# Kernel optimization log

Hardware: AMD Instinct MI355X
Metric: run time of the kernel (lower is better)

The kernel has to match this reference:

```python
import jax, jax.numpy as jnp
import numpy as np

N, E, F_IN, HID, G = 20000, 320000, 128, 128, 64
H, D = 8, 32  # TransformerConv heads, per-head dim


def setup_inputs() -> dict:
    key = jax.random.key(0)
    ks = jax.random.split(key, 24)
    def w(k, i, o):
        return (jax.random.normal(k, (i, o), jnp.float32) / np.float32(np.sqrt(i)))
    def b(k, o):
        return jax.random.normal(k, (o,), jnp.float32) * 0.01
    inp = {
        'x': jax.random.normal(ks[0], (N, F_IN), jnp.float32),
        'edge_index': jax.random.randint(ks[1], (2, E), 0, N, jnp.int32),
        'batch': jnp.sort(jax.random.randint(ks[2], (N,), 0, G, jnp.int32)),
        # SAGEConv 1: 128 -> 128 (lin_l has bias, lin_r none)
        's1_wl': w(ks[3], 128, 128), 's1_bl': b(ks[4], 128), 's1_wr': w(ks[5], 128, 128),
        # SAGEConv 2: 128 -> 256
        's2_wl': w(ks[6], 128, 256), 's2_bl': b(ks[7], 256), 's2_wr': w(ks[8], 128, 256),
        # TransformerConv 1: 256 -> 8*32
        't1_wq': w(ks[9], 256, 256), 't1_bq': b(ks[10], 256),
        't1_wk': w(ks[11], 256, 256), 't1_bk': b(ks[12], 256),
        't1_wv': w(ks[13], 256, 256), 't1_bv': b(ks[14], 256),
        't1_ws': w(ks[15], 256, 256), 't1_bs': b(ks[16], 256),
        # TransformerConv 2
        't2_wq': w(ks[17], 256, 256), 't2_bq': b(ks[18], 256),
        't2_wk': w(ks[19], 256, 256), 't2_bk': b(ks[20], 256),
        't2_wv': w(ks[21], 256, 256), 't2_bv': b(ks[22], 256),
        't2_ws': w(ks[23], 256, 256), 't2_bs': b(jax.random.fold_in(key, 100), 256),
        # proj MLP: 256 -> 512 -> HID
        'p1_w': w(jax.random.fold_in(key, 101), 256, 512), 'p1_b': b(jax.random.fold_in(key, 102), 512),
        'p2_w': w(jax.random.fold_in(key, 103), 512, HID), 'p2_b': b(jax.random.fold_in(key, 104), HID),
    }
    return inp


def _sage(x, src, dst, wl, bl, wr):
    # PyG SAGEConv (aggr='mean'): lin_l(mean_j x_j) + lin_r(x_i)
    s = jax.ops.segment_sum(x[src], dst, num_segments=N)           # [N,F]
    cnt = jax.ops.segment_sum(jnp.ones((src.shape[0], 1), x.dtype), dst, num_segments=N)
    mean = s / jnp.maximum(cnt, 1.0)
    return mean @ wl + bl + x @ wr


def _tconv(x, src, dst, wq, bq, wk, bk, wv, bv, ws, bs):
    # PyG TransformerConv(256, 32, heads=8): per-edge attention + skip
    q = (x @ wq + bq).reshape(N, H, D)
    k = (x @ wk + bk).reshape(N, H, D)
    v = (x @ wv + bv).reshape(N, H, D)
    logits = jnp.einsum('ehd,ehd->eh', q[dst], k[src]) / np.float32(np.sqrt(D))  # [E,H]
    m = jax.ops.segment_max(logits, dst, num_segments=N)           # [N,H]
    p = jnp.exp(logits - m[dst])
    denom = jax.ops.segment_sum(p, dst, num_segments=N)
    p = p / denom[dst]                                              # softmax per target node per head
    agg = jax.ops.segment_sum(p[:, :, None] * v[src], dst, num_segments=N)  # [N,H,D]
    return agg.reshape(N, H * D) + x @ ws + bs


def reference(x, edge_index, batch, s1_wl, s1_bl, s1_wr, s2_wl, s2_bl, s2_wr,
              t1_wq, t1_bq, t1_wk, t1_bk, t1_wv, t1_bv, t1_ws, t1_bs,
              t2_wq, t2_bq, t2_wk, t2_bk, t2_wv, t2_bv, t2_ws, t2_bs,
              p1_w, p1_b, p2_w, p2_b):
    src, dst = edge_index[0], edge_index[1]
    h = jax.nn.relu(_sage(x, src, dst, s1_wl, s1_bl, s1_wr))
    h = jax.nn.relu(_sage(h, src, dst, s2_wl, s2_bl, s2_wr))
    h = jax.nn.relu(_tconv(h, src, dst, t1_wq, t1_bq, t1_wk, t1_bk, t1_wv, t1_bv, t1_ws, t1_bs))
    h = jax.nn.relu(_tconv(h, src, dst, t2_wq, t2_bq, t2_wk, t2_bk, t2_wv, t2_bv, t2_ws, t2_bs))
    # proj: ReLU -> Linear(256,512) -> ReLU -> Linear(512,HID) -> Sigmoid
    h = jax.nn.relu(h)
    h = jax.nn.relu(h @ p1_w + p1_b)
    h = jax.nn.sigmoid(h @ p2_w + p2_b)
    return jax.ops.segment_max(h, batch, num_segments=G)            # global_max_pool [G,HID]
```

## Files before the change

kernel.cpp:

```cpp
#include <hip/hip_runtime.h>
#include <hip/hip_bf16.h>
#include <hip/hip_fp16.h>
#include <math.h>

#define NN 20000
#define EE 320000
#define GG 64
#define CH 16

typedef __hip_bfloat16 bf16;
typedef __attribute__((ext_vector_type(8))) short short8;
typedef __attribute__((ext_vector_type(4))) float f32x4;
typedef __attribute__((ext_vector_type(4))) unsigned int uint4v;
typedef __attribute__((ext_vector_type(2))) unsigned int uint2v;
typedef __attribute__((ext_vector_type(2))) _Float16 half2v;
typedef unsigned int uint;
typedef unsigned short ushort;

__device__ __forceinline__ float bfr2f(ushort u) {
    union { uint i; float f; } c; c.i = ((uint)u) << 16; return c.f;
}
__device__ __forceinline__ ushort f2bfr(float f) {
    bf16 h = __float2bfloat16(f);
    return *(ushort*)&h;
}

__device__ __forceinline__ float dot2acc(uint a, uint b, float c) {
#if __has_builtin(__builtin_amdgcn_fdot2)
    return __builtin_amdgcn_fdot2(__builtin_bit_cast(half2v, a),
                                  __builtin_bit_cast(half2v, b), c, false);
#else
    half2v ha = __builtin_bit_cast(half2v, a);
    half2v hb = __builtin_bit_cast(half2v, b);
    return c + (float)ha.x * (float)hb.x + (float)ha.y * (float)hb.y;
#endif
}

__device__ __forceinline__ void load_lds16(const void* g, void* l) {
    __builtin_amdgcn_global_load_lds(
        (const __attribute__((address_space(1))) unsigned int*)g,
        (__attribute__((address_space(3))) unsigned int*)l, 16, 0, 0);
}

#define PREP_CONV  1250
#define PREP_TP    (PREP_CONV + 800)
#define PREP_BIAS  (PREP_TP + 8)
#define PREP_OUTZ  (PREP_BIAS + 32)
#define PREP_COUNT (PREP_OUTZ + 1250)

__global__ __launch_bounds__(256) void prep_kernel(
    const float* x, bf16* xm1,
    const float* s1_wr, const float* s1_wl, const float* s2_wr, const float* s2_wl,
    const float* t1_wq, const float* t1_wk, const float* t1_wv, const float* t1_ws,
    const float* t2_wq, const float* t2_wk, const float* t2_wv, const float* t2_ws,
    const float* p1_w, const float* p2_w,
    bf16* w1cat, bf16* w2cat, bf16* qw1, bf16* qw2, bf16* p1t, bf16* p2t,
    const float* b1q, const float* b1k, const float* b1v, const float* b1s,
    const float* b2q, const float* b2k, const float* b2v, const float* b2s,
    float* qb1, float* qb2,
    float* pool_out,
    const int* dst, int* cnt) {
    __shared__ float tile[32][33];
    int bid = blockIdx.x;
    int tid = threadIdx.x;
    if (bid < PREP_CONV) {
        int g = bid * 256 + tid;
        int row = g >> 4;
        int col = (g & 15) * 8;
        f32x4 a = *(const f32x4*)(x + (size_t)row * 128 + col);
        f32x4 b = *(const f32x4*)(x + (size_t)row * 128 + col + 4);
        short8 v;
        v[0] = (short)f2bfr(a.x); v[1] = (short)f2bfr(a.y);
        v[2] = (short)f2bfr(a.z); v[3] = (short)f2bfr(a.w);
        v[4] = (short)f2bfr(b.x); v[5] = (short)f2bfr(b.y);
        v[6] = (short)f2bfr(b.z); v[7] = (short)f2bfr(b.w);
        *(short8*)(xm1 + (size_t)row * 256 + col) = v;
    } else if (bid < PREP_TP) {
        int tb = bid - PREP_CONV;
        const float* W; bf16* Wt; int KW, NW, KT, KO, lt;
        const float* t1w[4] = {t1_wq, t1_wk, t1_wv, t1_ws};
        const float* t2w[4] = {t2_wq, t2_wk, t2_wv, t2_ws};
        if (tb < 16)       { W = s1_wr; Wt = w1cat; KW = 128; NW = 128; KT = 256; KO = 0;   lt = tb; }
        else if (tb < 32)  { W = s1_wl; Wt = w1cat; KW = 128; NW = 128; KT = 256; KO = 128; lt = tb - 16; }
        else if (tb < 64)  { W = s2_wr; Wt = w2cat; KW = 128; NW = 256; KT = 256; KO = 0;   lt = tb - 32; }
        else if (tb < 96)  { W = s2_wl; Wt = w2cat; KW = 128; NW = 256; KT = 256; KO = 128; lt = tb - 64; }
        else if (tb < 352) { int m = (tb - 96) >> 6;  W = t1w[m]; Wt = qw1 + m * 65536; KW = 256; NW = 256; KT = 256; KO = 0; lt = (tb - 96) & 63; }
        else if (tb < 608) { int m = (tb - 352) >> 6; W = t2w[m]; Wt = qw2 + m * 65536; KW = 256; NW = 256; KT = 256; KO = 0; lt = (tb - 352) & 63; }
        else if (tb < 736) { W = p1_w; Wt = p1t; KW = 256; NW = 512; KT = 256; KO = 0; lt = tb - 608; }
        else               { W = p2_w; Wt = p2t; KW = 512; NW = 128; KT = 512; KO = 0; lt = tb - 736; }
        int ntiles_n = NW >> 5;
        int k0 = (lt / ntiles_n) * 32;
        int n0 = (lt % ntiles_n) * 32;
        int tx = tid & 31, ty = tid >> 5;
        #pragma unroll
        for (int r = 0; r < 4; r++)
            tile[ty + 8 * r][tx] = W[(size_t)(k0 + ty + 8 * r) * NW + n0 + tx];
        __syncthreads();
        #pragma unroll
        for (int r = 0; r < 4; r++)
            Wt[(size_t)(n0 + ty + 8 * r) * KT + KO + k0 + tx] =
                __float2bfloat16(tile[tx][ty + 8 * r]);
    } else if (bid < PREP_BIAS) {
        int i = (bid - PREP_TP) * 256 + tid;
        if (i < 2048) {
            float* d = (i < 1024) ? qb1 : qb2;
            int j = i & 1023;
            const float* s;
            if (i < 1024) s = (j < 256) ? b1q : (j < 512) ? b1k : (j < 768) ? b1v : b1s;
            else          s = (j < 256) ? b2q : (j < 512) ? b2k : (j < 768) ? b2v : b2s;
            d[j] = s[j & 255];
        }
    } else if (bid < PREP_OUTZ) {
        int i = (bid - PREP_BIAS) * 256 + tid;
        if (i < GG * 128) pool_out[i] = 0.f;
    } else {
        int e = (bid - PREP_OUTZ) * 256 + tid;
        if (e < EE) atomicAdd(&cnt[dst[e]], 1);
    }
}

__global__ __launch_bounds__(1024) void scan_kernel(int* __restrict__ cnt,
                                                    int* __restrict__ off, int n) {
    __shared__ int wsum[16];
    __shared__ int carry_s;
    int tid = threadIdx.x;
    int lane = tid & 63, wid = tid >> 6;
    if (tid == 0) { carry_s = 0; off[0] = 0; }
    __syncthreads();
    for (int base = 0; base < n; base += 1024) {
        int idx = base + tid;
        int val = (idx < n) ? cnt[idx] : 0;
        int x = val;
        #pragma unroll
        for (int s = 1; s < 64; s <<= 1) {
            int y = __shfl_up(x, s, 64);
            if (lane >= s) x += y;
        }
        if (lane == 63) wsum[wid] = x;
        __syncthreads();
        if (tid == 0) {
            int c = carry_s;
            #pragma unroll
            for (int w = 0; w < 16; w++) { int t = wsum[w]; wsum[w] = c; c += t; }
            carry_s = c;
        }
        __syncthreads();
        int incl = wsum[wid] + x;
        if (idx < n) {
            off[idx + 1] = incl;
            cnt[idx] = incl - val;
        }
        __syncthreads();
    }
}

__global__ __launch_bounds__(256) void fill_kernel(const int* __restrict__ src,
                                                   const int* __restrict__ dst,
                                                   int* __restrict__ cursor,
                                                   int* __restrict__ csr_src, int E) {
    int e = blockIdx.x * 256 + threadIdx.x;
    if (e < E) {
        int p = atomicAdd(&cursor[dst[e]], 1);
        csr_src[p] = src[e];
    }
}

__global__ __launch_bounds__(256) void mean2_kernel(const bf16* __restrict__ x, int xstride,
                                                    const int* __restrict__ off,
                                                    const int* __restrict__ csr_src,
                                                    bf16* __restrict__ outp, int ostride) {
    int node = blockIdx.x * 4 + (threadIdx.x >> 6);
    int l = threadIdx.x & 63;
    int el = l >> 5;
    int dp = l & 31;
    int e0 = off[node], e1 = off[node + 1];
    float s0 = 0.f, s1 = 0.f, s2 = 0.f, s3 = 0.f;
    for (int e = e0; e < e1; e += 8) {
        uint2v a[4];
        #pragma unroll
        for (int j = 0; j < 4; j++) {
            int ee = e + j * 2 + el;
            int sa = csr_src[min(ee, e1 - 1)];
            uint2v v = *(const uint2v*)(x + (size_t)sa * xstride + dp * 4);
            uint m = (ee < e1) ? 0xffffffffu : 0u;
            a[j].x = v.x & m;
            a[j].y = v.y & m;
        }
        #pragma unroll
        for (int j = 0; j < 4; j++) {
            union { uint i; float f; } t;
            t.i = a[j].x << 16;         s0 += t.f;
            t.i = a[j].x & 0xffff0000u; s1 += t.f;
            t.i = a[j].y << 16;         s2 += t.f;
            t.i = a[j].y & 0xffff0000u; s3 += t.f;
        }
    }
    s0 += __shfl_xor(s0, 32);
    s1 += __shfl_xor(s1, 32);
    s2 += __shfl_xor(s2, 32);
    s3 += __shfl_xor(s3, 32);
    if (el == 0) {
        int deg = e1 - e0;
        float inv = (deg > 0) ? 1.f / (float)deg : 0.f;
        uint2v r;
        r.x = ((uint)f2bfr(s1 * inv) << 16) | (uint)f2bfr(s0 * inv);
        r.y = ((uint)f2bfr(s3 * inv) << 16) | (uint)f2bfr(s2 * inv);
        *(uint2v*)(outp + (size_t)node * ostride + dp * 4) = r;
    }
}

template <int MODE, int TM>
__global__ __launch_bounds__(256, (TM == 128) ? 4 : 5)
void gemm_kernel(const bf16* __restrict__ A,
                 const bf16* __restrict__ Wt,
                 const float* __restrict__ bias,
                 void* __restrict__ Cv,
                 int M, int K, int N, int cstride,
                 const int* __restrict__ batch,
                 float* __restrict__ pool_out) {
    constexpr int NT = (TM == 128) ? 4 : 2;
    constexpr int CSTR = 136;
    union SMem {
        struct { short As[TM * 64]; short Bs[128 * 64]; } st;
        ushort ctile[TM * CSTR];
    };
    __shared__ SMem sm;
    __shared__ int bat[TM];
    int t = threadIdx.x;
    int lane = t & 63;
    int wave = t >> 6;
    int wm = (TM == 128) ? (wave >> 1) * 64 : 0;
    int wn = (TM == 128) ? (wave & 1) * 64 : wave * 32;
    int bm = blockIdx.y * TM, bn = blockIdx.x * 128;
    int quad = lane >> 4, l16 = lane & 15;
    int srow = t >> 3;
    int sc8  = t & 7;
    int scol = sc8 * 8;
    int gcol = (sc8 ^ (srow & 7)) * 8;
    int sw   = l16 & 7;

    if (MODE == 4 && t < TM) bat[t] = batch[min(bm + t, M - 1)];

    f32x4 acc[4][NT];
    f32x4 zero = {0.f, 0.f, 0.f, 0.f};
    #pragma unroll
    for (int i = 0; i < 4; i++)
        #pragma unroll
        for (int j = 0; j < NT; j++) acc[i][j] = zero;

    for (int kk = 0; kk < K; kk += 64) {
        #pragma unroll
        for (int r = 0; r < TM / 32; r++) {
            int row = r * 32 + srow;
            int gm = bm + row; gm = (gm < M) ? gm : (M - 1);
            load_lds16(A + (size_t)gm * K + kk + gcol, &sm.st.As[row * 64 + scol]);
        }
        #pragma unroll
        for (int r = 0; r < 4; r++) {
            int row = r * 32 + srow;
            load_lds16(Wt + (size_t)(bn + row) * K + kk + gcol, &sm.st.Bs[row * 64 + scol]);
        }
        __syncthreads();
        #pragma unroll
        for (int ks = 0; ks < 2; ks++) {
            short8 af[4], bfr[NT];
            #pragma unroll
            for (int i = 0; i < 4; i++)
                af[i] = *(const short8*)&sm.st.As[(wm + i * 16 + l16) * 64 + ((ks * 4 + quad) ^ sw) * 8];
            #pragma unroll
            for (int j = 0; j < NT; j++)
                bfr[j] = *(const short8*)&sm.st.Bs[(wn + j * 16 + l16) * 64 + ((ks * 4 + quad) ^ sw) * 8];
            #pragma unroll
            for (int i = 0; i < 4; i++)
                #pragma unroll
                for (int j = 0; j < NT; j++)
                    acc[i][j] = __builtin_amdgcn_mfma_f32_16x16x32_bf16(af[i], bfr[j], acc[i][j], 0, 0, 0);
        }
        __syncthreads();
    }

    if (MODE == 4) {
        int g0 = bat[0], gL = bat[TM - 1];
        #pragma unroll
        for (int j = 0; j < NT; j++) {
            int gn = bn + wn + j * 16 + l16;
            float m0 = 0.f, m1 = 0.f;
            #pragma unroll
            for (int i = 0; i < 4; i++) {
                #pragma unroll
                for (int r = 0; r < 4; r++) {
                    int row = i * 16 + quad * 4 + r;
                    int gm = bm + row;
                    if (gm >= M) continue;
                    float v = acc[i][j][r] + bias[gn];
                    v = 1.f / (1.f + expf(-v));
                    int g = bat[row];
                    if (g == g0) m0 = fmaxf(m0, v);
                    else if (g == gL) m1 = fmaxf(m1, v);
                    else atomicMax((int*)&pool_out[g * 128 + gn], __float_as_int(v));
                }
            }
            m0 = fmaxf(m0, __shfl_xor(m0, 16));
            m0 = fmaxf(m0, __shfl_xor(m0, 32));
            m1 = fmaxf(m1, __shfl_xor(m1, 16));
            m1 = fmaxf(m1, __shfl_xor(m1, 32));
            if (quad == 0) {
                atomicMax((int*)&pool_out[g0 * 128 + gn], __float_as_int(m0));
                if (gL != g0)
                    atomicMax((int*)&pool_out[gL * 128 + gn], __float_as_int(m1));
            }
        }
        return;
    }

    #pragma unroll
    for (int i = 0; i < 4; i++) {
        int row0 = wm + i * 16 + quad * 4;
        #pragma unroll
        for (int j = 0; j < NT; j++) {
            int col = wn + j * 16 + l16;
            int gn = bn + col;
            #pragma unroll
            for (int r = 0; r < 4; r++) {
                float v = acc[i][j][r] + bias[gn];
                if (MODE == 2) v = fmaxf(v, 0.f);
                ushort st;
                if (MODE == 5 && gn < 512) {
                    __half hh = __float2half(v);
                    st = *(ushort*)&hh;
                } else {
                    st = f2bfr(v);
                }
                sm.ctile[(row0 + r) * CSTR + col] = st;
            }
        }
    }
    __syncthreads();

    int orow = t >> 4;
    int ocol = (t & 15) * 8;
    #pragma unroll
    for (int rb = 0; rb < TM / 16; rb++) {
        int row = rb * 16 + orow;
        int gm = bm + row;
        if (gm < M) {
            short8 val = *(const short8*)&sm.ctile[row * CSTR + ocol];
            *(short8*)((ushort*)Cv + (size_t)gm * cstride + bn + ocol) = val;
        }
    }
}

template <int MODE, int TM>
static void launch_gemm(const bf16* A, const bf16* Wt, const float* bias, void* C,
                        int M, int K, int N, int cstride, hipStream_t st,
                        const int* batch = nullptr, float* pool_out = nullptr) {
    dim3 grid(N / 128, (M + TM - 1) / TM);
    hipLaunchKernelGGL((gemm_kernel<MODE, TM>), grid, dim3(256), 0, st,
                       A, Wt, bias, C, M, K, N, cstride, batch, pool_out);
}

__global__ __launch_bounds__(256) void attn5_kernel(const bf16* __restrict__ qkvs,
                                                    const int* __restrict__ off,
                                                    const int* __restrict__ csr_src,
                                                    bf16* __restrict__ out, int ostride) {
    __shared__ float pp[2][CH][9];
    __shared__ int srcs[2][CH];
    int i = blockIdx.x;
    int tid = threadIdx.x;
    int ea = tid >> 4, ha = (tid >> 1) & 7, half = tid & 1;
    int hc = tid >> 5, dp = (tid >> 1) & 15, epar = tid & 1;

    uint q2[8];
    {
        const uint4v* qp = (const uint4v*)(qkvs + (size_t)i * 1024 + ha * 32 + half * 16);
        uint4v a = qp[0], b = qp[1];
        q2[0] = a.x; q2[1] = a.y; q2[2] = a.z; q2[3] = a.w;
        q2[4] = b.x; q2[5] = b.y; q2[6] = b.z; q2[7] = b.w;
    }

    int e0 = off[i], e1 = off[i + 1];
    float l = 0.f, acc0 = 0.f, acc1 = 0.f;
    int vcol = 512 + hc * 32 + dp * 2;
    if (e0 < e1) {
        if (tid < CH) srcs[0][tid] = csr_src[min(e0 + tid, e1 - 1)];
        __syncthreads();
        int buf = 0;
        for (int base = e0; base < e1; base += CH, buf ^= 1) {
            int cnt = min(CH, e1 - base);
            uint vv[8];
            #pragma unroll
            for (int j = 0; j < 8; j++) {
                int e = epar + j * 2;
                vv[j] = *(const uint*)(qkvs + (size_t)srcs[buf][e] * 1024 + vcol);
            }
            int s = srcs[buf][ea];
            const uint4v* kp = (const uint4v*)(qkvs + (size_t)s * 1024 + 256 + ha * 32 + half * 16);
            uint4v ka = kp[0], kb = kp[1];
            if (tid < CH) srcs[buf ^ 1][tid] = csr_src[min(base + CH + tid, e1 - 1)];
            float d = 0.f;
            d = dot2acc(q2[0], ka.x, d); d = dot2acc(q2[1], ka.y, d);
            d = dot2acc(q2[2], ka.z, d); d = dot2acc(q2[3], ka.w, d);
            d = dot2acc(q2[4], kb.x, d); d = dot2acc(q2[5], kb.y, d);
            d = dot2acc(q2[6], kb.z, d); d = dot2acc(q2[7], kb.w, d);
            d += __shfl_xor(d, 1);
            float p = (ea < cnt) ? __expf(d * 0.17677669529663687f) : 0.f;
            if (half == 0) pp[buf][ea][ha] = p;
            __syncthreads();
            #pragma unroll
            for (int j = 0; j < 8; j++) {
                int e = epar + j * 2;
                float pj = pp[buf][e][hc];
                l += pj;
                union { uint i; float f; } lo, hi;
                lo.i = vv[j] << 16; hi.i = vv[j] & 0xffff0000u;
                acc0 += pj * lo.f;
                acc1 += pj * hi.f;
            }
        }
    }
    acc0 += __shfl_xor(acc0, 1);
    acc1 += __shfl_xor(acc1, 1);
    l    += __shfl_xor(l, 1);
    float inv = (l > 0.f) ? 1.f / l : 0.f;
    float r0 = acc0 * inv, r1 = acc1 * inv;
    if (epar == 0) {
        uint su = *(const uint*)(qkvs + (size_t)i * 1024 + 768 + hc * 32 + dp * 2);
        union { uint i; float f; } lo, hi;
        lo.i = su << 16; hi.i = su & 0xffff0000u;
        float v0 = fmaxf(r0 + lo.f, 0.f);
        float v1 = fmaxf(r1 + hi.f, 0.f);
        uint packed = ((uint)f2bfr(v1) << 16) | (uint)f2bfr(v0);
        *(uint*)(out + (size_t)i * ostride + hc * 32 + dp * 2) = packed;
    }
}

extern "C" void kernel_launch(void* const* d_in, const int* in_sizes, int n_in,
                              void* d_out, int out_size, void* d_ws, size_t ws_size,
                              hipStream_t stream) {
    const float* x      = (const float*)d_in[0];
    const int*   ei     = (const int*)d_in[1];
    const int*   batch  = (const int*)d_in[2];
    const float* s1_wl  = (const float*)d_in[3];
    const float* s1_bl  = (const float*)d_in[4];
    const float* s1_wr  = (const float*)d_in[5];
    const float* s2_wl  = (const float*)d_in[6];
    const float* s2_bl  = (const float*)d_in[7];
    const float* s2_wr  = (const float*)d_in[8];
    const float* t1_wq  = (const float*)d_in[9];
    const float* t1_bq  = (const float*)d_in[10];
    const float* t1_wk  = (const float*)d_in[11];
    const float* t1_bk  = (const float*)d_in[12];
    const float* t1_wv  = (const float*)d_in[13];
    const float* t1_bv  = (const float*)d_in[14];
    const float* t1_ws  = (const float*)d_in[15];
    const float* t1_bs  = (const float*)d_in[16];
    const float* t2_wq  = (const float*)d_in[17];
    const float* t2_bq  = (const float*)d_in[18];
    const float* t2_wk  = (const float*)d_in[19];
    const float* t2_bk  = (const float*)d_in[20];
    const float* t2_wv  = (const float*)d_in[21];
    const float* t2_bv  = (const float*)d_in[22];
    const float* t2_wsk = (const float*)d_in[23];
    const float* t2_bs  = (const float*)d_in[24];
    const float* p1_w   = (const float*)d_in[25];
    const float* p1_b   = (const float*)d_in[26];
    const float* p2_w   = (const float*)d_in[27];
    const float* p2_b   = (const float*)d_in[28];
    float* out = (float*)d_out;

    char* ws = (char*)d_ws;
    size_t o = 0;
    auto alloc = [&](size_t bytes) { char* p = ws + o; o += (bytes + 255) & ~(size_t)255; return p; };
    int* off     = (int*)alloc(sizeof(int) * (NN + 1));
    int* cursor  = (int*)alloc(sizeof(int) * NN);
    int* csr_src = (int*)alloc(sizeof(int) * EE);
    bf16* w1cat = (bf16*)alloc(2 * 128 * 256);
    bf16* w2cat = (bf16*)alloc(2 * 256 * 256);
    bf16* qw1   = (bf16*)alloc(2 * 1024 * 256);
    bf16* qw2   = (bf16*)alloc(2 * 1024 * 256);
    bf16* p1t   = (bf16*)alloc(2 * 512 * 256);
    bf16* p2t   = (bf16*)alloc(2 * 128 * 512);
    float* qb1  = (float*)alloc(4 * 1024);
    float* qb2  = (float*)alloc(4 * 1024);
    bf16* xm1   = (bf16*)alloc(2 * (size_t)NN * 256);
    bf16* xm2   = (bf16*)alloc(2 * (size_t)NN * 256);
    bf16* t1b   = (bf16*)alloc(2 * (size_t)NN * 512);
    bf16* Q     = (bf16*)alloc(2 * (size_t)NN * 1024);
    bf16* h2   = xm1;
    bf16* t1   = t1b;
    bf16* h4   = xm1;
    bf16* p1o  = t1b;

    const int* src = ei;
    const int* dst = ei + EE;

    hipMemsetAsync(cursor, 0, sizeof(int) * NN, stream);

    prep_kernel<<<PREP_COUNT, 256, 0, stream>>>(
        x, xm1,
        s1_wr, s1_wl, s2_wr, s2_wl,
        t1_wq, t1_wk, t1_wv, t1_ws,
        t2_wq, t2_wk, t2_wv, t2_wsk,
        p1_w, p2_w,
        w1cat, w2cat, qw1, qw2, p1t, p2t,
        t1_bq, t1_bk, t1_bv, t1_bs,
        t2_bq, t2_bk, t2_bv, t2_bs,
        qb1, qb2,
        out,
        dst, cursor);

    scan_kernel<<<1, 1024, 0, stream>>>(cursor, off, NN);
    fill_kernel<<<(EE + 255) / 256, 256, 0, stream>>>(src, dst, cursor, csr_src, EE);

    mean2_kernel<<<NN / 4, 256, 0, stream>>>(xm1, 256, off, csr_src, xm1 + 128, 256);
    launch_gemm<2, 64>(xm1, w1cat, s1_bl, xm2, NN, 256, 128, 256, stream);

    mean2_kernel<<<NN / 4, 256, 0, stream>>>(xm2, 256, off, csr_src, xm2 + 128, 256);
    launch_gemm<2, 64>(xm2, w2cat, s2_bl, h2, NN, 256, 256, 256, stream);

    launch_gemm<5, 128>(h2, qw1, qb1, Q, NN, 256, 1024, 1024, stream);
    attn5_kernel<<<NN, 256, 0, stream>>>(Q, off, csr_src, t1, 256);

    launch_gemm<5, 128>(t1, qw2, qb2, Q, NN, 256, 1024, 1024, stream);
    attn5_kernel<<<NN, 256, 0, stream>>>(Q, off, csr_src, h4, 256);

    launch_gemm<2, 128>(h4, p1t, p1_b, p1o, NN, 256, 512, 512, stream);
    launch_gemm<4, 64>(p1o, p2t, p2_b, nullptr, NN, 512, 128, 128, stream, batch, out);
}
```

Baseline: 374.1 us.

## Fuse projection MLP GEMMs and max-pool into one kernel keeping hidden in LDS

The two projection GEMMs (256->512 with ReLU, then 512->128 with sigmoid and global max-pool) are replaced by a single kernel. Each 32-row block keeps its 512-wide hidden activations in LDS, so the intermediate never goes to global memory and one launch is saved. In exchange the tiles are small (32 rows), every block reloads all of both weight matrices, and there is no double buffering, so the MFMA work may run less efficiently than in the larger-tile GEMM. The fused kernel indexes batch without a bounds check, which is safe only because 20000 is divisible by 32.

```diff
diff --git a/kernel.cpp b/kernel.cpp
--- a/kernel.cpp
+++ b/kernel.cpp
@@ -215,9 +215,7 @@
                  const bf16* __restrict__ Wt,
                  const float* __restrict__ bias,
                  void* __restrict__ Cv,
-                 int M, int K, int N, int cstride,
-                 const int* __restrict__ batch,
-                 float* __restrict__ pool_out) {
+                 int M, int K, int N, int cstride) {
     constexpr int NT = (TM == 128) ? 4 : 2;
     constexpr int CSTR = 136;
     union SMem {
@@ -225,7 +223,6 @@
         ushort ctile[TM * CSTR];
     };
     __shared__ SMem sm;
-    __shared__ int bat[TM];
     int t = threadIdx.x;
     int lane = t & 63;
     int wave = t >> 6;
@@ -239,8 +236,6 @@
     int gcol = (sc8 ^ (srow & 7)) * 8;
     int sw   = l16 & 7;
 
-    if (MODE == 4 && t < TM) bat[t] = batch[min(bm + t, M - 1)];
-
     f32x4 acc[4][NT];
     f32x4 zero = {0.f, 0.f, 0.f, 0.f};
     #pragma unroll
@@ -277,40 +272,6 @@
                     acc[i][j] = __builtin_amdgcn_mfma_f32_16x16x32_bf16(af[i], bfr[j], acc[i][j], 0, 0, 0);
         }
         __syncthreads();
-    }
-
-    if (MODE == 4) {
-        int g0 = bat[0], gL = bat[TM - 1];
-        #pragma unroll
-        for (int j = 0; j < NT; j++) {
-            int gn = bn + wn + j * 16 + l16;
-            float m0 = 0.f, m1 = 0.f;
-            #pragma unroll
-            for (int i = 0; i < 4; i++) {
-                #pragma unroll
-                for (int r = 0; r < 4; r++) {
-                    int row = i * 16 + quad * 4 + r;
-                    int gm = bm + row;
-                    if (gm >= M) continue;
-                    float v = acc[i][j][r] + bias[gn];
-                    v = 1.f / (1.f + expf(-v));
-                    int g = bat[row];
-                    if (g == g0) m0 = fmaxf(m0, v);
-                    else if (g == gL) m1 = fmaxf(m1, v);
-                    else atomicMax((int*)&pool_out[g * 128 + gn], __float_as_int(v));
-                }
-            }
-            m0 = fmaxf(m0, __shfl_xor(m0, 16));
-            m0 = fmaxf(m0, __shfl_xor(m0, 32));
-            m1 = fmaxf(m1, __shfl_xor(m1, 16));
-            m1 = fmaxf(m1, __shfl_xor(m1, 32));
-            if (quad == 0) {
-                atomicMax((int*)&pool_out[g0 * 128 + gn], __float_as_int(m0));
-                if (gL != g0)
-                    atomicMax((int*)&pool_out[gL * 128 + gn], __float_as_int(m1));
-            }
-        }
-        return;
     }
 
     #pragma unroll
@@ -352,11 +313,152 @@
 
 template <int MODE, int TM>
 static void launch_gemm(const bf16* A, const bf16* Wt, const float* bias, void* C,
-                        int M, int K, int N, int cstride, hipStream_t st,
-                        const int* batch = nullptr, float* pool_out = nullptr) {
+                        int M, int K, int N, int cstride, hipStream_t st) {
     dim3 grid(N / 128, (M + TM - 1) / TM);
     hipLaunchKernelGGL((gemm_kernel<MODE, TM>), grid, dim3(256), 0, st,
-                       A, Wt, bias, C, M, K, N, cstride, batch, pool_out);
+                       A, Wt, bias, C, M, K, N, cstride);
+}
+
+__global__ __launch_bounds__(256, 2) void fused_mlp_kernel(
+    const bf16* __restrict__ A,
+    const bf16* __restrict__ p1t,
+    const float* __restrict__ b1,
+    const bf16* __restrict__ p2t,
+    const float* __restrict__ b2,
+    const int* __restrict__ batch,
+    float* __restrict__ pool_out) {
+    constexpr int HSTR = 520;
+    __shared__ short As[32 * 64];
+    __shared__ short Bs[128 * 64];
+    __shared__ ushort hbuf[32 * HSTR];
+    __shared__ int bat[32];
+    int t = threadIdx.x;
+    int lane = t & 63;
+    int wave = t >> 6;
+    int wn = wave * 32;
+    int bm = blockIdx.x * 32;
+    int quad = lane >> 4, l16 = lane & 15;
+    int srow = t >> 3;
+    int sc8  = t & 7;
+    int scol = sc8 * 8;
+    int gcolA = (sc8 ^ (srow & 7)) * 8;
+    int srowB = t >> 3;
+    int sw = l16 & 7;
+
+    if (t < 32) bat[t] = batch[bm + t];
+
+    for (int p = 0; p < 4; p++) {
+        f32x4 acc[2][2];
+        f32x4 zero = {0.f, 0.f, 0.f, 0.f};
+        #pragma unroll
+        for (int i = 0; i < 2; i++)
+            #pragma unroll
+            for (int j = 0; j < 2; j++) acc[i][j] = zero;
+        for (int kk = 0; kk < 256; kk += 64) {
+            load_lds16(A + (size_t)(bm + srow) * 256 + kk + gcolA, &As[srow * 64 + scol]);
+            #pragma unroll
+            for (int r = 0; r < 4; r++) {
+                int row = r * 32 + srowB;
+                int grow = p * 128 + row;
+                load_lds16(p1t + (size_t)grow * 256 + kk + ((sc8 ^ (row & 7)) * 8),
+                           &Bs[row * 64 + scol]);
+            }
+            __syncthreads();
+            #pragma unroll
+            for (int ks = 0; ks < 2; ks++) {
+                short8 af[2], bfr[2];
+                #pragma unroll
+                for (int i = 0; i < 2; i++)
+                    af[i] = *(const short8*)&As[(i * 16 + l16) * 64 + ((ks * 4 + quad) ^ sw) * 8];
+                #pragma unroll
+                for (int j = 0; j < 2; j++)
+                    bfr[j] = *(const short8*)&Bs[(wn + j * 16 + l16) * 64 + ((ks * 4 + quad) ^ sw) * 8];
+                #pragma unroll
+                for (int i = 0; i < 2; i++)
+                    #pragma unroll
+                    for (int j = 0; j < 2; j++)
+                        acc[i][j] = __builtin_amdgcn_mfma_f32_16x16x32_bf16(af[i], bfr[j], acc[i][j], 0, 0, 0);
+            }
+            __syncthreads();
+        }
+        #pragma unroll
+        for (int i = 0; i < 2; i++) {
+            int row0 = i * 16 + quad * 4;
+            #pragma unroll
+            for (int j = 0; j < 2; j++) {
+                int col = p * 128 + wn + j * 16 + l16;
+                float bj = b1[col];
+                #pragma unroll
+                for (int r = 0; r < 4; r++) {
+                    float v = fmaxf(acc[i][j][r] + bj, 0.f);
+                    hbuf[(row0 + r) * HSTR + col] = f2bfr(v);
+                }
+            }
+        }
+    }
+
+    f32x4 acc2[2][2];
+    {
+        f32x4 zero = {0.f, 0.f, 0.f, 0.f};
+        #pragma unroll
+        for (int i = 0; i < 2; i++)
+            #pragma unroll
+            for (int j = 0; j < 2; j++) acc2[i][j] = zero;
+    }
+    for (int kk = 0; kk < 512; kk += 64) {
+        #pragma unroll
+        for (int r = 0; r < 4; r++) {
+            int row = r * 32 + srowB;
+            load_lds16(p2t + (size_t)row * 512 + kk + ((sc8 ^ (row & 7)) * 8),
+                       &Bs[row * 64 + scol]);
+        }
+        __syncthreads();
+        #pragma unroll
+        for (int ks = 0; ks < 2; ks++) {
+            short8 af[2], bfr[2];
+            #pragma unroll
+            for (int i = 0; i < 2; i++)
+                af[i] = *(const short8*)&hbuf[(i * 16 + l16) * HSTR + kk + ks * 32 + quad * 8];
+            #pragma unroll
+            for (int j = 0; j < 2; j++)
+                bfr[j] = *(const short8*)&Bs[(wn + j * 16 + l16) * 64 + ((ks * 4 + quad) ^ sw) * 8];
+            #pragma unroll
+            for (int i = 0; i < 2; i++)
+                #pragma unroll
+                for (int j = 0; j < 2; j++)
+                    acc2[i][j] = __builtin_amdgcn_mfma_f32_16x16x32_bf16(af[i], bfr[j], acc2[i][j], 0, 0, 0);
+        }
+        __syncthreads();
+    }
+    int g0 = bat[0], gL = bat[31];
+    #pragma unroll
+    for (int j = 0; j < 2; j++) {
+        int gn = wn + j * 16 + l16;
+        float bj = b2[gn];
+        float m0 = 0.f, m1 = 0.f;
+        #pragma unroll
+        for (int i = 0; i < 2; i++) {
+            #pragma unroll
+            for (int r = 0; r < 4; r++) {
+                int row = i * 16 + quad * 4 + r;
+                float v = acc2[i][j][r] + bj;
+                v = 1.f / (1.f + expf(-v));
+                int g = bat[row];
+                if (g == g0) m0 = fmaxf(m0, v);
+                else if (g == gL) m1 = fmaxf(m1, v);
+                else atomicMax((int*)&pool_out[g * 128 + gn], __float_as_int(v));
+            }
+        }
+        m0 = fmaxf(m0, __shfl_xor(m0, 16));
+        m0 = fmaxf(m0, __shfl_xor(m0, 32));
+        m1 = fmaxf(m1, __shfl_xor(m1, 16));
+        m1 = fmaxf(m1, __shfl_xor(m1, 32));
+        if (quad == 0) {
+            atomicMax((int*)&pool_out[g0 * 128 + gn], __float_as_int(m0));
+            if (gL != g0)
+                atomicMax((int*)&pool_out[gL * 128 + gn], __float_as_int(m1));
+        }
+    }
 }
 
 __global__ __launch_bounds__(256) void attn5_kernel(const bf16* __restrict__ qkvs,
@@ -489,7 +591,6 @@
     bf16* h2   = xm1;
     bf16* t1   = t1b;
     bf16* h4   = xm1;
-    bf16* p1o  = t1b;
 
     const int* src = ei;
     const int* dst = ei + EE;
@@ -524,6 +625,5 @@
     launch_gemm<5, 128>(t1, qw2, qb2, Q, NN, 256, 1024, 1024, stream);
     attn5_kernel<<<NN, 256, 0, stream>>>(Q, off, csr_src, h4, 256);
 
-    launch_gemm<2, 128>(h4, p1t, p1_b, p1o, NN, 256, 512, 512, stream);
-    launch_gemm<4, 64>(p1o, p2t, p2_b, nullptr, NN, 512, 128, 128, stream, batch, out);
-}
+    fused_mlp_kernel<<<NN / 32, 256, 0, stream>>>(h4, p1t, p1_b, p2t, p2_b, batch, out);
+}
```

Result: no change. 374.5 us (+0.1%).
